# Optimization experiments

Hardware: AMD Instinct MI355X
Metric: run time of the kernel (lower is better)

The kernel has to match this reference:

```python
import jax, jax.numpy as jnp
import numpy as np

MARGIN = 1.0
N, D, P = 4096, 768, 100

def setup_inputs() -> dict:
    key = jax.random.key(0)
    k1, k2, k3 = jax.random.split(key, 3)
    inputs = jax.random.normal(k1, (N, D), dtype=jnp.float32)
    targets = jax.random.randint(k2, (N,), 0, P)
    center = jax.random.normal(k3, (P, D), dtype=jnp.float32)
    return {"inputs": inputs, "targets": targets, "center": center}

def reference(inputs, targets, center):
    n = inputs.shape[0]
    # pairwise euclidean distances: ||xi||^2 + ||xj||^2 - 2 xi.xj
    sq = jnp.sum(inputs * inputs, axis=1)                      # [n]
    dist = sq[:, None] + sq[None, :] - 2.0 * (inputs @ inputs.T)
    dist = jnp.sqrt(jnp.clip(dist, 1e-12))                     # [n, n]
    mask = targets[:, None] == targets[None, :]                # same-class mask
    inf = jnp.asarray(jnp.inf, dist.dtype)
    # hardest positive: max over same-class (diagonal always True -> finite)
    dist_ap = jnp.max(jnp.where(mask, dist, -inf), axis=1)     # [n]
    # hardest negative: min over different-class, fallback ap+margin if none
    dist_an = jnp.min(jnp.where(mask, inf, dist), axis=1)      # [n]
    has_neg = jnp.any(~mask, axis=1)
    dist_an = jnp.where(has_neg, dist_an, dist_ap + MARGIN)
    # prototype augmentation: row-normalized centers, min distance to any center
    cn = center / jnp.linalg.norm(center, axis=1, keepdims=True)
    csq = jnp.sum(cn * cn, axis=1)                             # [P]
    d2c = sq[:, None] + csq[None, :] - 2.0 * (inputs @ cn.T)   # [n, P]
    d2c = jnp.clip(jnp.sqrt(jnp.clip(d2c, 0.0)), 1e-12)
    dist_an = jnp.minimum(dist_an, jnp.min(d2c, axis=1))
    # MarginRankingLoss(dist_an, dist_ap, y=1) = mean(relu(margin - (an - ap)))
    return jnp.mean(jax.nn.relu(MARGIN + dist_ap - dist_an))
```

## Files before the change

### kernel.cpp

```cpp
#include <hip/hip_runtime.h>
#include <math.h>

#define N_ 4096
#define D_ 768
#define P_ 100
#define PPAD 128
#define NT 24
#define NTRI 528
#define NBLK 560

typedef __attribute__((ext_vector_type(8))) short short8;
typedef __attribute__((ext_vector_type(4))) float f32x4;

typedef const __attribute__((address_space(1))) void* gld_src_t;
typedef __attribute__((address_space(3))) void* gld_dst_t;
#define GLOAD16(g, d) __builtin_amdgcn_global_load_lds((gld_src_t)(g), (gld_dst_t)(d), 16, 0, 0)

#define WAITVM4() asm volatile("s_waitcnt vmcnt(4)" ::: "memory")
#define WAITVM0() asm volatile("s_waitcnt vmcnt(0)" ::: "memory")
#define WAITLGKM0() asm volatile("s_waitcnt lgkmcnt(0)" ::: "memory")

__device__ inline unsigned short f2bf(float f) {
    union { float f; unsigned int u; } v; v.f = f;
    unsigned int u = v.u + 0x7fffu + ((v.u >> 16) & 1u);
    return (unsigned short)(u >> 16);
}

static __device__ __forceinline__ void decode_tile(int orig, int* pit, int* pjt) {
    const int x = orig & 7;
    const int k = orig >> 3;
    if (k >= 66) { *pit = x * 4 + (k - 66); *pjt = 32; return; }
    const int g = x * 66 + k;
    const int cumR[11] = {0, 36, 100, 136, 200, 264, 300, 364, 428, 492, 528};
    const int GIr[10] = {0, 1, 1, 2, 2, 2, 3, 3, 3, 3};
    const int GJr[10] = {0, 0, 1, 0, 1, 2, 0, 1, 2, 3};
    int r = 0;
    while (cumR[r + 1] <= g) ++r;
    const int u = g - cumR[r];
    int di, dj;
    if (GIr[r] == GJr[r]) {
        di = 0;
        while ((di + 1) * (di + 2) / 2 <= u) ++di;
        dj = u - di * (di + 1) / 2;
    } else {
        di = u >> 3; dj = u & 7;
    }
    *pit = GIr[r] * 8 + di;
    *pjt = GJr[r] * 8 + dj;
}

__global__ __launch_bounds__(256) void pre_kernel(
    const float* __restrict__ X, const float* __restrict__ C,
    float* __restrict__ sq, unsigned short* __restrict__ Xbf,
    unsigned short* __restrict__ cnbf, float* __restrict__ csq) {
    const int gw = blockIdx.x * 4 + (threadIdx.x >> 6);
    const int l = threadIdx.x & 63;
    if (gw < N_) {
        const float4* x4 = (const float4*)(X + (size_t)gw * D_);
        short4* ob = (short4*)(Xbf + (size_t)gw * D_);
        float s = 0.f;
#pragma unroll
        for (int c = 0; c < 3; ++c) {
            float4 v = x4[c * 64 + l];
            s = fmaf(v.x, v.x, fmaf(v.y, v.y, fmaf(v.z, v.z, fmaf(v.w, v.w, s))));
            short4 o;
            o.x = (short)f2bf(v.x); o.y = (short)f2bf(v.y);
            o.z = (short)f2bf(v.z); o.w = (short)f2bf(v.w);
            ob[c * 64 + l] = o;
        }
#pragma unroll
        for (int m = 1; m < 64; m <<= 1) s += __shfl_xor(s, m);
        if (l == 0) sq[gw] = s;
    } else {
        const int p = gw - N_;
        if (p >= PPAD) return;
        short4* ob = (short4*)(cnbf + (size_t)p * D_);
        if (p < P_) {
            const float4* c4 = (const float4*)(C + (size_t)p * D_);
            float4 v[3];
            float s = 0.f;
#pragma unroll
            for (int c = 0; c < 3; ++c) {
                v[c] = c4[c * 64 + l];
                s = fmaf(v[c].x, v[c].x, fmaf(v[c].y, v[c].y,
                    fmaf(v[c].z, v[c].z, fmaf(v[c].w, v[c].w, s))));
            }
#pragma unroll
            for (int m = 1; m < 64; m <<= 1) s += __shfl_xor(s, m);
            float rn = 1.0f / sqrtf(s);
#pragma unroll
            for (int c = 0; c < 3; ++c) {
                short4 o;
                o.x = (short)f2bf(v[c].x * rn); o.y = (short)f2bf(v[c].y * rn);
                o.z = (short)f2bf(v[c].z * rn); o.w = (short)f2bf(v[c].w * rn);
                ob[c * 64 + l] = o;
            }
            if (l == 0) csq[p] = s * rn * rn;
        } else {
            short4 z; z.x = z.y = z.z = z.w = 0;
#pragma unroll
            for (int c = 0; c < 3; ++c) ob[c * 64 + l] = z;
            if (l == 0) csq[p] = 1e30f;
        }
    }
}

__global__ __launch_bounds__(256, 3) void mfma_kernel(
    const unsigned short* __restrict__ Xbf, const unsigned short* __restrict__ cnbf,
    const int* __restrict__ T, const float* __restrict__ sq,
    const float* __restrict__ csq,
    float* __restrict__ ap_part, float* __restrict__ an_part,
    float* __restrict__ minc) {
    __shared__ __align__(16) unsigned short lds[3 * 8192];

    const int tid = threadIdx.x;
    const int l = tid & 63;
    const int w = tid >> 6;
    const int wr = w >> 1;
    const int wc = w & 1;

    int it, jt;
    decode_tile(blockIdx.x, &it, &jt);
    const bool is_center = (jt == 32);
    const int i0 = it * 128;
    const int j0 = is_center ? 0 : jt * 128;
    const unsigned short* __restrict__ Bmat = is_center ? cnbf : Xbf;

    const int srow = tid >> 2;
    const int scol = ((tid & 3) * 8) ^ (((srow & 6) >> 1) << 3);
    const unsigned short* gA0 = Xbf + (size_t)(i0 + srow) * D_ + scol;
    const unsigned short* gA1 = gA0 + (size_t)64 * D_;
    const unsigned short* gB0 = Bmat + (size_t)(j0 + srow) * D_ + scol;
    const unsigned short* gB1 = gB0 + (size_t)64 * D_;
    const int dA0 = w * 512, dA1 = 2048 + w * 512;
    const int dB0 = 4096 + w * 512, dB1 = 6144 + w * 512;

    const int col = l & 15;
    const int hi = l >> 4;
    const int rko = (hi * 8) ^ ((l & 6) << 2);
    const int aro = (wr * 64 + col) * 32 + rko;
    const int bro = 4096 + (wc * 64 + col) * 32 + rko;

    f32x4 acc[4][4];
#pragma unroll
    for (int m = 0; m < 4; ++m)
#pragma unroll
        for (int n = 0; n < 4; ++n) acc[m][n] = (f32x4){0.f, 0.f, 0.f, 0.f};

#define STAGE(t)                                                     \
    do {                                                             \
        const int bo_ = ((t) % 3) * 8192;                            \
        const int ke_ = (t) * 32;                                    \
        GLOAD16(gA0 + ke_, &lds[bo_ + dA0]);                         \
        GLOAD16(gA1 + ke_, &lds[bo_ + dA1]);                         \
        GLOAD16(gB0 + ke_, &lds[bo_ + dB0]);                         \
        GLOAD16(gB1 + ke_, &lds[bo_ + dB1]);                         \
    } while (0)

    STAGE(0);
    STAGE(1);
    WAITVM4();
    __builtin_amdgcn_s_barrier();
    __builtin_amdgcn_sched_barrier(0);

    int bo = 0;
#pragma unroll 3
    for (int t = 0; t < NT; ++t) {
        const unsigned short* Lb = &lds[bo * 8192];
        short8 a[4], b[4];
#pragma unroll
        for (int m = 0; m < 4; ++m)
            a[m] = *reinterpret_cast<const short8*>(Lb + aro + m * 512);
#pragma unroll
        for (int n = 0; n < 4; ++n)
            b[n] = *reinterpret_cast<const short8*>(Lb + bro + n * 512);
        if (t + 2 < NT) STAGE(t + 2);
        WAITLGKM0();
        if (t < NT - 1) {
            if (t + 2 < NT) WAITVM4();
            else WAITVM0();
            __builtin_amdgcn_s_barrier();
            __builtin_amdgcn_sched_barrier(0);
        }
#pragma unroll
        for (int m = 0; m < 4; ++m)
#pragma unroll
            for (int n = 0; n < 4; ++n)
                acc[m][n] = __builtin_amdgcn_mfma_f32_16x16x32_bf16(
                    a[m], b[n], acc[m][n], 0, 0, 0);
        bo = (bo == 2) ? 0 : bo + 1;
    }
#undef STAGE

    float* lf = (float*)lds;
    __syncthreads();

    if (!is_center) {
        float sqj[4]; int tj[4];
#pragma unroll
        for (int n = 0; n < 4; ++n) {
            int j = j0 + wc * 64 + n * 16 + col;
            sqj[n] = sq[j];
            tj[n] = T[j];
        }
        float apC[4], anC[4];
#pragma unroll
        for (int n = 0; n < 4; ++n) { apC[n] = -1e30f; anC[n] = 1e30f; }

#pragma unroll
        for (int m = 0; m < 4; ++m) {
#pragma unroll
            for (int r = 0; r < 4; ++r) {
                const int lrow = wr * 64 + m * 16 + hi * 4 + r;
                const int i = i0 + lrow;
                float sqi = sq[i];
                int ti = T[i];
                float apR = -1e30f, anR = 1e30f;
#pragma unroll
                for (int n = 0; n < 4; ++n) {
                    float d2 = sqi + sqj[n] - 2.0f * acc[m][n][r];
                    float d = sqrtf(fmaxf(d2, 1e-12f));
                    bool same = (tj[n] == ti);
                    apR = same ? fmaxf(apR, d) : apR;
                    anR = same ? anR : fminf(anR, d);
                    apC[n] = same ? fmaxf(apC[n], d) : apC[n];
                    anC[n] = same ? anC[n] : fminf(anC[n], d);
                }
#pragma unroll
                for (int msk = 1; msk < 16; msk <<= 1) {
                    apR = fmaxf(apR, __shfl_xor(apR, msk));
                    anR = fminf(anR, __shfl_xor(anR, msk));
                }
                if (col == 0) {
                    lf[wc * 128 + lrow] = apR;
                    lf[256 + wc * 128 + lrow] = anR;
                }
            }
        }
        __syncthreads();
        if (tid < 128) {
            float a = fmaxf(lf[tid], lf[128 + tid]);
            float b = fminf(lf[256 + tid], lf[384 + tid]);
            ap_part[(size_t)jt * N_ + i0 + tid] = a;
            an_part[(size_t)jt * N_ + i0 + tid] = b;
        }

        if (it != jt) {
            __syncthreads();
#pragma unroll
            for (int n = 0; n < 4; ++n) {
                apC[n] = fmaxf(apC[n], __shfl_xor(apC[n], 16));
                apC[n] = fmaxf(apC[n], __shfl_xor(apC[n], 32));
                anC[n] = fminf(anC[n], __shfl_xor(anC[n], 16));
                anC[n] = fminf(anC[n], __shfl_xor(anC[n], 32));
                if (hi == 0) {
                    int jl = wc * 64 + n * 16 + col;
                    lf[wr * 128 + jl] = apC[n];
                    lf[256 + wr * 128 + jl] = anC[n];
                }
            }
            __syncthreads();
            if (tid < 128) {
                float a = fmaxf(lf[tid], lf[128 + tid]);
                float b = fminf(lf[256 + tid], lf[384 + tid]);
                ap_part[(size_t)(32 + it) * N_ + j0 + tid] = a;
                an_part[(size_t)(32 + it) * N_ + j0 + tid] = b;
            }
        }
    } else {
        float sqj[4];
#pragma unroll
        for (int n = 0; n < 4; ++n) sqj[n] = csq[wc * 64 + n * 16 + col];
#pragma unroll
        for (int m = 0; m < 4; ++m) {
#pragma unroll
            for (int r = 0; r < 4; ++r) {
                const int lrow = wr * 64 + m * 16 + hi * 4 + r;
                const int i = i0 + lrow;
                float sqi = sq[i];
                float mc = 1e30f;
#pragma unroll
                for (int n = 0; n < 4; ++n) {
                    float d2 = sqi + sqj[n] - 2.0f * acc[m][n][r];
                    float d = fmaxf(sqrtf(fmaxf(d2, 0.0f)), 1e-12f);
                    mc = fminf(mc, d);
                }
#pragma unroll
                for (int msk = 1; msk < 16; msk <<= 1)
                    mc = fminf(mc, __shfl_xor(mc, msk));
                if (col == 0) lf[wc * 128 + lrow] = mc;
            }
        }
        __syncthreads();
        if (tid < 128) minc[i0 + tid] = fminf(lf[tid], lf[128 + tid]);
    }
}

__global__ __launch_bounds__(256) void combine2(
    const float* __restrict__ ap_part, const float* __restrict__ an_part,
    const float* __restrict__ minc, float* __restrict__ bsum) {
    const int w = threadIdx.x >> 6;
    const int l = threadIdx.x & 63;
    const int l2 = l & 31;
    float wsum = 0.f;
#pragma unroll
    for (int q = 0; q < 4; ++q) {
        const int i = blockIdx.x * 16 + w * 4 + q;
        const int r = i >> 7;
        const int s = (l2 <= r) ? l2 : 32 + l2;
        float v = (l < 32) ? ap_part[(size_t)s * N_ + i]
                           : an_part[(size_t)s * N_ + i];
#pragma unroll
        for (int m = 1; m < 32; m <<= 1) {
            float o = __shfl_xor(v, m);
            v = (l < 32) ? fmaxf(v, o) : fminf(v, o);
        }
        float ap = __shfl(v, 0);
        float an = __shfl(v, 32);
        float dan = (an < 1e29f) ? an : (ap + 1.0f);
        dan = fminf(dan, minc[i]);
        wsum += fmaxf(0.0f, 1.0f + ap - dan);
    }
    if (l == 0) bsum[blockIdx.x * 4 + w] = wsum;
}

__global__ __launch_bounds__(256) void finalize(
    const float* __restrict__ bsum, float* __restrict__ out) {
    __shared__ float sred[4];
    const int tid = threadIdx.x;
    float s = bsum[tid] + bsum[tid + 256] + bsum[tid + 512] + bsum[tid + 768];
#pragma unroll
    for (int m = 32; m > 0; m >>= 1) s += __shfl_xor(s, m);
    if ((tid & 63) == 0) sred[tid >> 6] = s;
    __syncthreads();
    if (tid == 0)
        out[0] = (sred[0] + sred[1] + sred[2] + sred[3]) / (float)N_;
}

extern "C" void kernel_launch(void* const* d_in, const int* in_sizes, int n_in,
                              void* d_out, int out_size, void* d_ws, size_t ws_size,
                              hipStream_t stream) {
    const float* X = (const float*)d_in[0];
    const int* T = (const int*)d_in[1];
    const float* C = (const float*)d_in[2];
    float* out = (float*)d_out;

    float* ws = (float*)d_ws;
    float* sq = ws;
    float* csq = ws + 4096;
    float* minc = ws + 4224;
    float* bsum = ws + 8320;
    unsigned short* Xbf = (unsigned short*)(ws + 9344);
    unsigned short* cnbf = (unsigned short*)(ws + 1582208);
    float* ap_part = ws + 1631360;
    float* an_part = ws + 1893504;

    pre_kernel<<<(N_ + PPAD) / 4, 256, 0, stream>>>(X, C, sq, Xbf, cnbf, csq);
    mfma_kernel<<<NBLK, 256, 0, stream>>>(Xbf, cnbf, T, sq, csq, ap_part, an_part, minc);
    combine2<<<N_ / 16, 256, 0, stream>>>(ap_part, an_part, minc, bsum);
    finalize<<<1, 256, 0, stream>>>(bsum, out);
}
```

Measured before the change: 50.79 us.

## Fuse finalize into combine via last-block atomic, reorder staging, skip diag column work

Merges the finalize kernel into the combine kernel using a global atomic counter, so the last block performs the final reduction; the counter is reset in pre_kernel. This removes one kernel launch. The global-to-LDS prefetch is now issued before the LDS fragment reads in the MFMA loop, and diagonal tiles skip the column-wise ap/an accumulation they never use. The risks are ordering between the atomic and the fences, and a possible change in how the loads and MFMAs overlap.

```diff
diff --git a/kernel.cpp b/kernel.cpp
--- a/kernel.cpp
+++ b/kernel.cpp
@@ -52,7 +52,9 @@
 __global__ __launch_bounds__(256) void pre_kernel(
     const float* __restrict__ X, const float* __restrict__ C,
     float* __restrict__ sq, unsigned short* __restrict__ Xbf,
-    unsigned short* __restrict__ cnbf, float* __restrict__ csq) {
+    unsigned short* __restrict__ cnbf, float* __restrict__ csq,
+    int* __restrict__ sync) {
+    if (blockIdx.x == 0 && threadIdx.x == 0) sync[0] = 0;
     const int gw = blockIdx.x * 4 + (threadIdx.x >> 6);
     const int l = threadIdx.x & 63;
     if (gw < N_) {
@@ -122,6 +124,7 @@
     int it, jt;
     decode_tile(blockIdx.x, &it, &jt);
     const bool is_center = (jt == 32);
+    const bool is_diag = (!is_center) && (it == jt);
     const int i0 = it * 128;
     const int j0 = is_center ? 0 : jt * 128;
     const unsigned short* __restrict__ Bmat = is_center ? cnbf : Xbf;
@@ -166,6 +169,7 @@
     int bo = 0;
 #pragma unroll 3
     for (int t = 0; t < NT; ++t) {
+        if (t + 2 < NT) STAGE(t + 2);
         const unsigned short* Lb = &lds[bo * 8192];
         short8 a[4], b[4];
 #pragma unroll
@@ -174,7 +178,6 @@
 #pragma unroll
         for (int n = 0; n < 4; ++n)
             b[n] = *reinterpret_cast<const short8*>(Lb + bro + n * 512);
-        if (t + 2 < NT) STAGE(t + 2);
         WAITLGKM0();
         if (t < NT - 1) {
             if (t + 2 < NT) WAITVM4();
@@ -223,8 +226,10 @@
                     bool same = (tj[n] == ti);
                     apR = same ? fmaxf(apR, d) : apR;
                     anR = same ? anR : fminf(anR, d);
-                    apC[n] = same ? fmaxf(apC[n], d) : apC[n];
-                    anC[n] = same ? anC[n] : fminf(anC[n], d);
+                    if (!is_diag) {
+                        apC[n] = same ? fmaxf(apC[n], d) : apC[n];
+                        anC[n] = same ? anC[n] : fminf(anC[n], d);
+                    }
                 }
 #pragma unroll
                 for (int msk = 1; msk < 16; msk <<= 1) {
@@ -245,7 +250,7 @@
             an_part[(size_t)jt * N_ + i0 + tid] = b;
         }
 
-        if (it != jt) {
+        if (!is_diag) {
             __syncthreads();
 #pragma unroll
             for (int n = 0; n < 4; ++n) {
@@ -296,11 +301,15 @@
     }
 }
 
-__global__ __launch_bounds__(256) void combine2(
+__global__ __launch_bounds__(256) void combine2f(
     const float* __restrict__ ap_part, const float* __restrict__ an_part,
-    const float* __restrict__ minc, float* __restrict__ bsum) {
-    const int w = threadIdx.x >> 6;
-    const int l = threadIdx.x & 63;
+    const float* __restrict__ minc, float* __restrict__ bsum,
+    float* __restrict__ out, int* __restrict__ sync) {
+    __shared__ float sred[4];
+    __shared__ int amlast;
+    const int tid = threadIdx.x;
+    const int w = tid >> 6;
+    const int l = tid & 63;
     const int l2 = l & 31;
     float wsum = 0.f;
 #pragma unroll
@@ -322,19 +331,20 @@
         wsum += fmaxf(0.0f, 1.0f + ap - dan);
     }
     if (l == 0) bsum[blockIdx.x * 4 + w] = wsum;
-}
-
-__global__ __launch_bounds__(256) void finalize(
-    const float* __restrict__ bsum, float* __restrict__ out) {
-    __shared__ float sred[4];
-    const int tid = threadIdx.x;
-    float s = bsum[tid] + bsum[tid + 256] + bsum[tid + 512] + bsum[tid + 768];
-#pragma unroll
-    for (int m = 32; m > 0; m >>= 1) s += __shfl_xor(s, m);
-    if ((tid & 63) == 0) sred[tid >> 6] = s;
+    __threadfence();
     __syncthreads();
-    if (tid == 0)
-        out[0] = (sred[0] + sred[1] + sred[2] + sred[3]) / (float)N_;
+    if (tid == 0) amlast = (atomicAdd(&sync[0], 1) == (N_ / 16) - 1);
+    __syncthreads();
+    if (amlast) {
+        __threadfence();
+        float s = bsum[tid] + bsum[tid + 256] + bsum[tid + 512] + bsum[tid + 768];
+#pragma unroll
+        for (int m = 32; m > 0; m >>= 1) s += __shfl_xor(s, m);
+        if (l == 0) sred[w] = s;
+        __syncthreads();
+        if (tid == 0)
+            out[0] = (sred[0] + sred[1] + sred[2] + sred[3]) / (float)N_;
+    }
 }
 
 extern "C" void kernel_launch(void* const* d_in, const int* in_sizes, int n_in,
@@ -354,9 +364,9 @@
     unsigned short* cnbf = (unsigned short*)(ws + 1582208);
     float* ap_part = ws + 1631360;
     float* an_part = ws + 1893504;
-
-    pre_kernel<<<(N_ + PPAD) / 4, 256, 0, stream>>>(X, C, sq, Xbf, cnbf, csq);
+    int* sync = (int*)(ws + 2155648);
+
+    pre_kernel<<<(N_ + PPAD) / 4, 256, 0, stream>>>(X, C, sq, Xbf, cnbf, csq, sync);
     mfma_kernel<<<NBLK, 256, 0, stream>>>(Xbf, cnbf, T, sq, csq, ap_part, an_part, minc);
-    combine2<<<N_ / 16, 256, 0, stream>>>(ap_part, an_part, minc, bsum);
-    finalize<<<1, 256, 0, stream>>>(bsum, out);
-}
+    combine2f<<<N_ / 16, 256, 0, stream>>>(ap_part, an_part, minc, bsum, out, sync);
+}
```

Result: slower. 66.95 us (+31.8%).
